# Kernel tuning notes

Measured on AMD Instinct MI355X. Metric: run time of the kernel, lower is better.

## Reference

```python
import jax, jax.numpy as jnp
import numpy as np

B, S, D_MODEL, N_HEADS = 4, 8192, 1024, 16
D_K = D_MODEL // N_HEADS


def setup_inputs() -> dict:
    key = jax.random.key(0)
    k1, k2, k3 = jax.random.split(key, 3)
    x = jax.random.normal(k1, (B, S, D_MODEL), dtype=jnp.float32)
    w_qkv = jax.random.normal(k2, (D_MODEL, 3 * D_MODEL), dtype=jnp.float32) * (1.0 / np.sqrt(D_MODEL))
    w_o = jax.random.normal(k3, (D_MODEL, D_MODEL), dtype=jnp.float32) * (1.0 / np.sqrt(D_MODEL))
    return {"x": x, "w_qkv": w_qkv, "w_o": w_o}


def reference(x, w_qkv, w_o):
    b, s, dm = x.shape
    h, d = N_HEADS, D_K
    qkv = (x @ w_qkv).reshape(b, s, 3, h, d)  # (b, s, 3, h, d)
    q, k, v = qkv[:, :, 0], qkv[:, :, 1], qkv[:, :, 2]  # each (b, s, h, d)
    # ELU+1 feature map (positive features)
    q = jax.nn.elu(q) + 1.0
    k = jax.nn.elu(k) + 1.0
    # Global (non-causal) KV aggregation: (b, h, d, d)
    kv = jnp.einsum('bnhd,bnhf->bhdf', k, v)
    k_sum = k.sum(axis=1)  # (b, h, d)
    numerator = jnp.einsum('bnhd,bhdf->bnhf', q, kv)  # (b, s, h, d)
    denominator = jnp.einsum('bnhd,bhd->bnh', q, k_sum)[..., None] + 1e-6
    attn = (numerator / denominator).reshape(b, s, dm)
    return attn @ w_o
```

## Files before the change

### kernel.cpp

```cpp
#include <hip/hip_runtime.h>
#include <cmath>

constexpr int BB = 4;
constexpr int SS = 8192;
constexpr int DMODEL = 1024;
constexpr int NHEADS = 16;
constexpr int DHEAD = 64;
constexpr int MTOK = BB * SS;

typedef __attribute__((ext_vector_type(8))) short short8;
typedef __attribute__((ext_vector_type(4))) float f32x4;

__device__ __forceinline__ unsigned short f2bf(float f) {
    unsigned u = __float_as_uint(f);
    u += 0x7FFF + ((u >> 16) & 1);
    return (unsigned short)(u >> 16);
}

#define STAGE2(gbase, lbase)                                                          \
    do {                                                                              \
        __builtin_amdgcn_global_load_lds(                                             \
            (const __attribute__((address_space(1))) unsigned int*)((gbase) + o0),    \
            (__attribute__((address_space(3))) unsigned int*)((lbase) + d0), 16, 0, 0);\
        __builtin_amdgcn_global_load_lds(                                             \
            (const __attribute__((address_space(1))) unsigned int*)((gbase) + o1),    \
            (__attribute__((address_space(3))) unsigned int*)((lbase) + d1), 16, 0, 0);\
    } while (0)

template <int EPI>
__global__ __launch_bounds__(512, 2) void la_gemm256(
    const unsigned short* __restrict__ A, const unsigned short* __restrict__ B,
    float* __restrict__ Cf,
    unsigned short* __restrict__ Cq, unsigned short* __restrict__ Ck,
    unsigned short* __restrict__ Cv,
    const int N, const int K, const int GX)
{
    extern __shared__ __align__(16) unsigned short smem[];

    const int t = threadIdx.x;
    const int wave = t >> 6, lane = t & 63;
    const int wm = wave >> 2, wn = wave & 3;
    const int quad = lane >> 4, fl = lane & 15;

    const int nwg = (int)gridDim.x;
    const int cpx = nwg >> 3;
    const int id = ((int)blockIdx.x & 7) * cpx + ((int)blockIdx.x >> 3);
    const int bx = id % GX, by = id / GX;
    const int m0 = by * 256, n0 = bx * 256;

    const unsigned short* a_g = A + (size_t)m0 * K;
    const unsigned short* b_g = B + (size_t)n0 * K;

    const int c0 = t, c1 = 512 + t;
    const size_t o0 = (size_t)(c0 >> 2) * K + (size_t)((((c0 & 3) ^ ((c0 >> 3) & 3))) << 3);
    const size_t o1 = (size_t)(c1 >> 2) * K + (size_t)((((c1 & 3) ^ ((c1 >> 3) & 3))) << 3);
    const int d0 = c0 * 8, d1 = c1 * 8;

    const int qsc = (quad ^ ((fl >> 1) & 3)) << 3;
    const int offA = (wm * 128 + fl) * 32 + qsc;
    const int offB = (wn * 64 + fl) * 32 + qsc;

    f32x4 acc[8][4];
#pragma unroll
    for (int i = 0; i < 8; ++i)
#pragma unroll
        for (int j = 0; j < 4; ++j) acc[i][j] = (f32x4){0.f, 0.f, 0.f, 0.f};

    unsigned short* bufc = smem;
    unsigned short* bufn = smem + 32768;

    STAGE2(a_g,      bufc);
    STAGE2(b_g,      bufc + 16384);
    STAGE2(a_g + 32, bufc + 8192);
    STAGE2(b_g + 32, bufc + 24576);
    asm volatile("s_waitcnt vmcnt(4)" ::: "memory");
    __builtin_amdgcn_s_barrier();

    for (int kt = 0; kt < K - 64; kt += 64) {
        const unsigned short* an = a_g + kt + 64;
        const unsigned short* bn = b_g + kt + 64;
        short8 ah[4], bh[4];

#pragma unroll
        for (int i = 0; i < 4; ++i) ah[i] = *(const short8*)(bufc + offA + i * 512);
#pragma unroll
        for (int j = 0; j < 4; ++j) bh[j] = *(const short8*)(bufc + 16384 + offB + j * 512);
        STAGE2(an, bufn);
        __builtin_amdgcn_s_barrier();
        asm volatile("s_waitcnt lgkmcnt(0)" ::: "memory");
        __builtin_amdgcn_s_setprio(1);
#pragma unroll
        for (int i = 0; i < 4; ++i)
#pragma unroll
            for (int j = 0; j < 4; ++j)
                acc[i][j] = __builtin_amdgcn_mfma_f32_16x16x32_bf16(ah[i], bh[j], acc[i][j], 0, 0, 0);
        __builtin_amdgcn_s_setprio(0);
        __builtin_amdgcn_s_barrier();

#pragma unroll
        for (int i = 0; i < 4; ++i) ah[i] = *(const short8*)(bufc + offA + 2048 + i * 512);
        STAGE2(bn, bufn + 16384);
        __builtin_amdgcn_s_barrier();
        asm volatile("s_waitcnt lgkmcnt(0)" ::: "memory");
        __builtin_amdgcn_s_setprio(1);
#pragma unroll
        for (int i = 0; i < 4; ++i)
#pragma unroll
            for (int j = 0; j < 4; ++j)
                acc[4 + i][j] = __builtin_amdgcn_mfma_f32_16x16x32_bf16(ah[i], bh[j], acc[4 + i][j], 0, 0, 0);
        __builtin_amdgcn_s_setprio(0);
        asm volatile("s_waitcnt vmcnt(4)" ::: "memory");
        __builtin_amdgcn_s_barrier();

#pragma unroll
        for (int i = 0; i < 4; ++i) ah[i] = *(const short8*)(bufc + 8192 + offA + i * 512);
#pragma unroll
        for (int j = 0; j < 4; ++j) bh[j] = *(const short8*)(bufc + 24576 + offB + j * 512);
        STAGE2(an + 32, bufn + 8192);
        __builtin_amdgcn_s_barrier();
        asm volatile("s_waitcnt lgkmcnt(0)" ::: "memory");
        __builtin_amdgcn_s_setprio(1);
#pragma unroll
        for (int i = 0; i < 4; ++i)
#pragma unroll
            for (int j = 0; j < 4; ++j)
                acc[i][j] = __builtin_amdgcn_mfma_f32_16x16x32_bf16(ah[i], bh[j], acc[i][j], 0, 0, 0);
        __builtin_amdgcn_s_setprio(0);
        __builtin_amdgcn_s_barrier();

#pragma unroll
        for (int i = 0; i < 4; ++i) ah[i] = *(const short8*)(bufc + 8192 + offA + 2048 + i * 512);
        STAGE2(bn + 32, bufn + 24576);
        __builtin_amdgcn_s_barrier();
        asm volatile("s_waitcnt lgkmcnt(0)" ::: "memory");
        __builtin_amdgcn_s_setprio(1);
#pragma unroll
        for (int i = 0; i < 4; ++i)
#pragma unroll
            for (int j = 0; j < 4; ++j)
                acc[4 + i][j] = __builtin_amdgcn_mfma_f32_16x16x32_bf16(ah[i], bh[j], acc[4 + i][j], 0, 0, 0);
        __builtin_amdgcn_s_setprio(0);
        asm volatile("s_waitcnt vmcnt(4)" ::: "memory");
        __builtin_amdgcn_s_barrier();

        unsigned short* tmp = bufc; bufc = bufn; bufn = tmp;
    }

    {
        short8 ah[4], bh[4];
#pragma unroll
        for (int i = 0; i < 4; ++i) ah[i] = *(const short8*)(bufc + offA + i * 512);
#pragma unroll
        for (int j = 0; j < 4; ++j) bh[j] = *(const short8*)(bufc + 16384 + offB + j * 512);
#pragma unroll
        for (int i = 0; i < 4; ++i)
#pragma unroll
            for (int j = 0; j < 4; ++j)
                acc[i][j] = __builtin_amdgcn_mfma_f32_16x16x32_bf16(ah[i], bh[j], acc[i][j], 0, 0, 0);
#pragma unroll
        for (int i = 0; i < 4; ++i) ah[i] = *(const short8*)(bufc + offA + 2048 + i * 512);
#pragma unroll
        for (int i = 0; i < 4; ++i)
#pragma unroll
            for (int j = 0; j < 4; ++j)
                acc[4 + i][j] = __builtin_amdgcn_mfma_f32_16x16x32_bf16(ah[i], bh[j], acc[4 + i][j], 0, 0, 0);
        asm volatile("s_waitcnt vmcnt(0)" ::: "memory");
        __builtin_amdgcn_s_barrier();
#pragma unroll
        for (int i = 0; i < 4; ++i) ah[i] = *(const short8*)(bufc + 8192 + offA + i * 512);
#pragma unroll
        for (int j = 0; j < 4; ++j) bh[j] = *(const short8*)(bufc + 24576 + offB + j * 512);
#pragma unroll
        for (int i = 0; i < 4; ++i)
#pragma unroll
            for (int j = 0; j < 4; ++j)
                acc[i][j] = __builtin_amdgcn_mfma_f32_16x16x32_bf16(ah[i], bh[j], acc[i][j], 0, 0, 0);
#pragma unroll
        for (int i = 0; i < 4; ++i) ah[i] = *(const short8*)(bufc + 8192 + offA + 2048 + i * 512);
#pragma unroll
        for (int i = 0; i < 4; ++i)
#pragma unroll
            for (int j = 0; j < 4; ++j)
                acc[4 + i][j] = __builtin_amdgcn_mfma_f32_16x16x32_bf16(ah[i], bh[j], acc[4 + i][j], 0, 0, 0);
    }

    if (EPI == 1) {
        const int bsel = n0 >> 10;
        unsigned short* Cp = (bsel == 0) ? Cq : ((bsel == 1) ? Ck : Cv);
        const bool act = (bsel < 2);
        const int colb = (n0 & 1023) + wn * 64 + fl;
#pragma unroll
        for (int i = 0; i < 8; ++i) {
            const int rowb = m0 + wm * 128 + i * 16 + quad * 4;
#pragma unroll
            for (int j = 0; j < 4; ++j) {
                const int col = colb + j * 16;
#pragma unroll
                for (int r = 0; r < 4; ++r) {
                    float v = acc[i][j][r];
                    if (act) v = (v > 0.f) ? v + 1.f : __expf(v);
                    Cp[(size_t)(rowb + r) * 1024 + col] = f2bf(v);
                }
            }
        }
    } else {
#pragma unroll
        for (int i = 0; i < 8; ++i) {
            const int rowb = m0 + wm * 128 + i * 16 + quad * 4;
#pragma unroll
            for (int j = 0; j < 4; ++j) {
                const int col = n0 + wn * 64 + fl + j * 16;
#pragma unroll
                for (int r = 0; r < 4; ++r)
                    Cf[(size_t)(rowb + r) * N + col] = acc[i][j][r];
            }
        }
    }
}

__global__ __launch_bounds__(256) void cast_bf16(
    const float4* __restrict__ in, ushort4* __restrict__ hi, int n4)
{
    int i = blockIdx.x * 256 + threadIdx.x;
    const int stride = gridDim.x * 256;
    for (; i < n4; i += stride) {
        const float4 v = in[i];
        ushort4 h;
        h.x = f2bf(v.x); h.y = f2bf(v.y); h.z = f2bf(v.z); h.w = f2bf(v.w);
        hi[i] = h;
    }
}

__global__ __launch_bounds__(256) void cast_T(
    const float* __restrict__ w, unsigned short* __restrict__ hiT, int Kd, int Nd)
{
    __shared__ float tile[32][33];
    const int t = threadIdx.x;
    const int n0 = blockIdx.x * 32, k0 = blockIdx.y * 32;
    const int r = t >> 3, c4 = (t & 7) * 4;
    const float4 v = *(const float4*)(w + (size_t)(k0 + r) * Nd + n0 + c4);
    tile[r][c4 + 0] = v.x; tile[r][c4 + 1] = v.y;
    tile[r][c4 + 2] = v.z; tile[r][c4 + 3] = v.w;
    __syncthreads();
    ushort4 h;
    h.x = f2bf(tile[c4 + 0][r]); h.y = f2bf(tile[c4 + 1][r]);
    h.z = f2bf(tile[c4 + 2][r]); h.w = f2bf(tile[c4 + 3][r]);
    *(ushort4*)(hiT + (size_t)(n0 + r) * Kd + k0 + c4) = h;
}

constexpr int KV_CHUNKS = 16;

__global__ __launch_bounds__(256) void la_kvsum(
    const unsigned short* __restrict__ Kb, const unsigned short* __restrict__ Vb,
    float* __restrict__ kv, float* __restrict__ ksum)
{
    __shared__ float kk[32][68];
    __shared__ float vv[32][68];
    const int t = threadIdx.x;
    const int bh = blockIdx.x;
    const int b = bh >> 4, h = bh & 15;
    const int r = t >> 3, c8 = (t & 7) * 8;
    const int d0 = (t & 15) * 4, f0 = (t >> 4) * 4;
    float acc[4][4];
#pragma unroll
    for (int i = 0; i < 4; ++i)
#pragma unroll
        for (int j = 0; j < 4; ++j) acc[i][j] = 0.f;
    float ks = 0.f;
    const int s0 = blockIdx.y * (SS / KV_CHUNKS);

    for (int st = 0; st < SS / KV_CHUNKS; st += 32) {
        const size_t row = (size_t)(b * SS + s0 + st + r) * DMODEL + h * DHEAD + c8;
        const uint4 ku = *(const uint4*)(Kb + row);
        const uint4 vu = *(const uint4*)(Vb + row);
        __syncthreads();
        const unsigned ka_[4] = {ku.x, ku.y, ku.z, ku.w};
        const unsigned va_[4] = {vu.x, vu.y, vu.z, vu.w};
#pragma unroll
        for (int e = 0; e < 4; ++e) {
            kk[r][c8 + 2 * e]     = __uint_as_float(ka_[e] << 16);
            kk[r][c8 + 2 * e + 1] = __uint_as_float(ka_[e] & 0xFFFF0000u);
            vv[r][c8 + 2 * e]     = __uint_as_float(va_[e] << 16);
            vv[r][c8 + 2 * e + 1] = __uint_as_float(va_[e] & 0xFFFF0000u);
        }
        __syncthreads();
#pragma unroll 8
        for (int rr = 0; rr < 32; ++rr) {
            float4 kr = *(const float4*)&kk[rr][d0];
            float4 vr = *(const float4*)&vv[rr][f0];
            float ka[4] = {kr.x, kr.y, kr.z, kr.w};
            float va[4] = {vr.x, vr.y, vr.z, vr.w};
#pragma unroll
            for (int i = 0; i < 4; ++i)
#pragma unroll
                for (int j = 0; j < 4; ++j)
                    acc[i][j] = fmaf(ka[i], va[j], acc[i][j]);
        }
        if (t < 64) {
#pragma unroll 8
            for (int rr = 0; rr < 32; ++rr) ks += kk[rr][t];
        }
    }

    float* kvp = kv + (size_t)bh * DHEAD * DHEAD;
#pragma unroll
    for (int i = 0; i < 4; ++i)
#pragma unroll
        for (int j = 0; j < 4; ++j)
            atomicAdd(&kvp[(d0 + i) * DHEAD + f0 + j], acc[i][j]);
    if (t < 64) atomicAdd(&ksum[bh * DHEAD + t], ks);
}

__global__ __launch_bounds__(256) void la_attn(
    const unsigned short* __restrict__ Q, const float* __restrict__ kv,
    const float* __restrict__ ksum, unsigned short* __restrict__ attn)
{
    __shared__ float kvs[64][68];
    __shared__ float qs[64][68];
    __shared__ float kss[64];
    const int t = threadIdx.x;
    const int t0 = blockIdx.x * 64;
    const int b = t0 / SS;
    const int tok_g = t >> 4;
    const int f_g = t & 15;

    for (int hh = 0; hh < NHEADS; ++hh) {
        __syncthreads();
        const float* kvp = kv + (size_t)(b * NHEADS + hh) * DHEAD * DHEAD;
#pragma unroll
        for (int i = 0; i < 4; ++i) {
            const int idx = i * 256 + t;
            const int r = idx >> 4, c4 = (idx & 15) * 4;
            *(float4*)&kvs[r][c4] = *(const float4*)(kvp + r * 64 + c4);
        }
        if (t < 64) kss[t] = ksum[(b * NHEADS + hh) * DHEAD + t];
#pragma unroll
        for (int i = 0; i < 2; ++i) {
            const int idx = i * 256 + t;
            const int r = idx >> 3, c8 = (idx & 7) * 8;
            const uint4 qu = *(const uint4*)(Q + (size_t)(t0 + r) * DMODEL + hh * 64 + c8);
            const unsigned a[4] = {qu.x, qu.y, qu.z, qu.w};
#pragma unroll
            for (int e = 0; e < 4; ++e) {
                qs[r][c8 + 2 * e]     = __uint_as_float(a[e] << 16);
                qs[r][c8 + 2 * e + 1] = __uint_as_float(a[e] & 0xFFFF0000u);
            }
        }
        __syncthreads();

        float acc[4][4];
        float den[4];
#pragma unroll
        for (int i = 0; i < 4; ++i) {
            den[i] = 0.f;
#pragma unroll
            for (int j = 0; j < 4; ++j) acc[i][j] = 0.f;
        }
#pragma unroll 8
        for (int d = 0; d < 64; ++d) {
            const float4 kvf = *(const float4*)&kvs[d][f_g * 4];
            const float ks = kss[d];
#pragma unroll
            for (int i = 0; i < 4; ++i) {
                const float qd = qs[tok_g * 4 + i][d];
                den[i]    = fmaf(qd, ks,    den[i]);
                acc[i][0] = fmaf(qd, kvf.x, acc[i][0]);
                acc[i][1] = fmaf(qd, kvf.y, acc[i][1]);
                acc[i][2] = fmaf(qd, kvf.z, acc[i][2]);
                acc[i][3] = fmaf(qd, kvf.w, acc[i][3]);
            }
        }
#pragma unroll
        for (int i = 0; i < 4; ++i) {
            const float rcp = 1.f / (den[i] + 1e-6f);
            ushort4 o;
            o.x = f2bf(acc[i][0] * rcp); o.y = f2bf(acc[i][1] * rcp);
            o.z = f2bf(acc[i][2] * rcp); o.w = f2bf(acc[i][3] * rcp);
            *(ushort4*)(attn + (size_t)(t0 + tok_g * 4 + i) * DMODEL + hh * 64 + f_g * 4) = o;
        }
    }
}

__global__ void la_sentinel(float* out, int n) {
    int i = blockIdx.x * 256 + threadIdx.x;
    if (i < n) out[i] = 12345.0f;
}

extern "C" void kernel_launch(void* const* d_in, const int* in_sizes, int n_in,
                              void* d_out, int out_size, void* d_ws, size_t ws_size,
                              hipStream_t stream)
{
    const float* x     = (const float*)d_in[0];
    const float* w_qkv = (const float*)d_in[1];
    const float* w_o   = (const float*)d_in[2];
    float* out = (float*)d_out;

    static bool attr_done = []() {
        hipFuncSetAttribute((const void*)&la_gemm256<1>,
                            hipFuncAttributeMaxDynamicSharedMemorySize, 131072);
        hipFuncSetAttribute((const void*)&la_gemm256<0>,
                            hipFuncAttributeMaxDynamicSharedMemorySize, 131072);
        return true;
    }();
    (void)attr_done;

    char* p = (char*)d_ws;
    const size_t x_bf = (size_t)MTOK * DMODEL * 2;
    unsigned short* x_hi = (unsigned short*)p; p += x_bf;
    unsigned short* wqT = (unsigned short*)p; p += (size_t)3 * DMODEL * DMODEL * 2;
    unsigned short* woT = (unsigned short*)p; p += (size_t)DMODEL * DMODEL * 2;
    unsigned short* q_buf = (unsigned short*)p; p += x_bf;
    unsigned short* k_buf = (unsigned short*)p; p += x_bf;
    unsigned short* v_buf = (unsigned short*)p; p += x_bf;
    float* kvb = (float*)p; p += (size_t)BB * NHEADS * DHEAD * DHEAD * 4;
    float* ksb = (float*)p; p += (size_t)BB * NHEADS * DHEAD * 4;

    if ((size_t)(p - (char*)d_ws) > ws_size) {
        la_sentinel<<<(MTOK * DMODEL + 255) / 256, 256, 0, stream>>>(out, MTOK * DMODEL);
        return;
    }

    hipMemsetAsync(kvb, 0,
                   (size_t)(BB * NHEADS * DHEAD * DHEAD + BB * NHEADS * DHEAD) * sizeof(float),
                   stream);

    cast_bf16<<<8192, 256, 0, stream>>>((const float4*)x, (ushort4*)x_hi,
                                        MTOK * DMODEL / 4);
    cast_T<<<dim3(3 * DMODEL / 32, DMODEL / 32), 256, 0, stream>>>(w_qkv, wqT,
                                                                   DMODEL, 3 * DMODEL);
    cast_T<<<dim3(DMODEL / 32, DMODEL / 32), 256, 0, stream>>>(w_o, woT,
                                                               DMODEL, DMODEL);

    la_gemm256<1><<<(3 * DMODEL / 256) * (MTOK / 256), 512, 131072, stream>>>(
        x_hi, wqT, nullptr, q_buf, k_buf, v_buf, 3 * DMODEL, DMODEL, 3 * DMODEL / 256);

    la_kvsum<<<dim3(BB * NHEADS, KV_CHUNKS), 256, 0, stream>>>(k_buf, v_buf, kvb, ksb);

    la_attn<<<MTOK / 64, 256, 0, stream>>>(q_buf, kvb, ksb, x_hi);

    la_gemm256<0><<<(DMODEL / 256) * (MTOK / 256), 512, 131072, stream>>>(
        x_hi, woT, out, nullptr, nullptr, nullptr, DMODEL, DMODEL, DMODEL / 256);
}
```

Baseline: 727.0 us.

## Double-buffer MFMA register fragments to overlap LDS reads with matrix math

Measured after the change: 719.2 us. No clear change (-1.1%).

```diff
diff --git a/kernel.cpp b/kernel.cpp
--- a/kernel.cpp
+++ b/kernel.cpp
@@ -27,6 +27,18 @@
             (__attribute__((address_space(3))) unsigned int*)((lbase) + d1), 16, 0, 0);\
     } while (0)
 
+#define MFMA16(ACCROW, AH, BH)                                                        \
+    do {                                                                              \
+        __builtin_amdgcn_s_setprio(1);                                                \
+        _Pragma("unroll")                                                             \
+        for (int i = 0; i < 4; ++i)                                                   \
+            _Pragma("unroll")                                                         \
+            for (int j = 0; j < 4; ++j)                                               \
+                acc[ACCROW + i][j] = __builtin_amdgcn_mfma_f32_16x16x32_bf16(         \
+                    AH[i], BH[j], acc[ACCROW + i][j], 0, 0, 0);                       \
+        __builtin_amdgcn_s_setprio(0);                                                \
+    } while (0)
+
 template <int EPI>
 __global__ __launch_bounds__(512, 2) void la_gemm256(
     const unsigned short* __restrict__ A, const unsigned short* __restrict__ B,
@@ -75,114 +87,54 @@
     STAGE2(b_g + 32, bufc + 24576);
     asm volatile("s_waitcnt vmcnt(4)" ::: "memory");
     __builtin_amdgcn_s_barrier();
-
-    for (int kt = 0; kt < K - 64; kt += 64) {
-        const unsigned short* an = a_g + kt + 64;
-        const unsigned short* bn = b_g + kt + 64;
-        short8 ah[4], bh[4];
-
-#pragma unroll
-        for (int i = 0; i < 4; ++i) ah[i] = *(const short8*)(bufc + offA + i * 512);
-#pragma unroll
-        for (int j = 0; j < 4; ++j) bh[j] = *(const short8*)(bufc + 16384 + offB + j * 512);
+    __builtin_amdgcn_sched_barrier(0);
+
+    short8 ah0[4], ah1[4], bh0[4], bh1[4];
+#pragma unroll
+    for (int i = 0; i < 4; ++i) ah0[i] = *(const short8*)(bufc + offA + i * 512);
+#pragma unroll
+    for (int j = 0; j < 4; ++j) bh0[j] = *(const short8*)(bufc + 16384 + offB + j * 512);
+
+    for (int kt = 0; kt < K; kt += 64) {
+        const int ktn = (kt + 64 < K) ? kt + 64 : kt;
+        const unsigned short* an = a_g + ktn;
+        const unsigned short* bn = b_g + ktn;
+
+#pragma unroll
+        for (int i = 0; i < 4; ++i) ah1[i] = *(const short8*)(bufc + offA + 2048 + i * 512);
         STAGE2(an, bufn);
+        MFMA16(0, ah0, bh0);
+        asm volatile("s_waitcnt vmcnt(2)" ::: "memory");
         __builtin_amdgcn_s_barrier();
-        asm volatile("s_waitcnt lgkmcnt(0)" ::: "memory");
-        __builtin_amdgcn_s_setprio(1);
-#pragma unroll
-        for (int i = 0; i < 4; ++i)
-#pragma unroll
-            for (int j = 0; j < 4; ++j)
-                acc[i][j] = __builtin_amdgcn_mfma_f32_16x16x32_bf16(ah[i], bh[j], acc[i][j], 0, 0, 0);
-        __builtin_amdgcn_s_setprio(0);
+        __builtin_amdgcn_sched_barrier(0);
+
+#pragma unroll
+        for (int i = 0; i < 4; ++i) ah0[i] = *(const short8*)(bufc + 8192 + offA + i * 512);
+#pragma unroll
+        for (int j = 0; j < 4; ++j) bh1[j] = *(const short8*)(bufc + 24576 + offB + j * 512);
+        STAGE2(bn, bufn + 16384);
+        MFMA16(4, ah1, bh0);
         __builtin_amdgcn_s_barrier();
 
 #pragma unroll
-        for (int i = 0; i < 4; ++i) ah[i] = *(const short8*)(bufc + offA + 2048 + i * 512);
-        STAGE2(bn, bufn + 16384);
+        for (int i = 0; i < 4; ++i) ah1[i] = *(const short8*)(bufc + 8192 + offA + 2048 + i * 512);
+        STAGE2(an + 32, bufn + 8192);
+        MFMA16(0, ah0, bh1);
+        asm volatile("s_waitcnt vmcnt(2)" ::: "memory");
         __builtin_amdgcn_s_barrier();
-        asm volatile("s_waitcnt lgkmcnt(0)" ::: "memory");
-        __builtin_amdgcn_s_setprio(1);
-#pragma unroll
-        for (int i = 0; i < 4; ++i)
-#pragma unroll
-            for (int j = 0; j < 4; ++j)
-                acc[4 + i][j] = __builtin_amdgcn_mfma_f32_16x16x32_bf16(ah[i], bh[j], acc[4 + i][j], 0, 0, 0);
-        __builtin_amdgcn_s_setprio(0);
-        asm volatile("s_waitcnt vmcnt(4)" ::: "memory");
+        __builtin_amdgcn_sched_barrier(0);
+
+#pragma unroll
+        for (int i = 0; i < 4; ++i) ah0[i] = *(const short8*)(bufn + offA + i * 512);
+#pragma unroll
+        for (int j = 0; j < 4; ++j) bh0[j] = *(const short8*)(bufn + 16384 + offB + j * 512);
+        STAGE2(bn + 32, bufn + 24576);
+        MFMA16(4, ah1, bh1);
         __builtin_amdgcn_s_barrier();
 
-#pragma unroll
-        for (int i = 0; i < 4; ++i) ah[i] = *(const short8*)(bufc + 8192 + offA + i * 512);
-#pragma unroll
-        for (int j = 0; j < 4; ++j) bh[j] = *(const short8*)(bufc + 24576 + offB + j * 512);
-        STAGE2(an + 32, bufn + 8192);
-        __builtin_amdgcn_s_barrier();
-        asm volatile("s_waitcnt lgkmcnt(0)" ::: "memory");
-        __builtin_amdgcn_s_setprio(1);
-#pragma unroll
-        for (int i = 0; i < 4; ++i)
-#pragma unroll
-            for (int j = 0; j < 4; ++j)
-                acc[i][j] = __builtin_amdgcn_mfma_f32_16x16x32_bf16(ah[i], bh[j], acc[i][j], 0, 0, 0);
-        __builtin_amdgcn_s_setprio(0);
-        __builtin_amdgcn_s_barrier();
-
-#pragma unroll
-        for (int i = 0; i < 4; ++i) ah[i] = *(const short8*)(bufc + 8192 + offA + 2048 + i * 512);
-        STAGE2(bn + 32, bufn + 24576);
-        __builtin_amdgcn_s_barrier();
-        asm volatile("s_waitcnt lgkmcnt(0)" ::: "memory");
-        __builtin_amdgcn_s_setprio(1);
-#pragma unroll
-        for (int i = 0; i < 4; ++i)
-#pragma unroll
-            for (int j = 0; j < 4; ++j)
-                acc[4 + i][j] = __builtin_amdgcn_mfma_f32_16x16x32_bf16(ah[i], bh[j], acc[4 + i][j], 0, 0, 0);
-        __builtin_amdgcn_s_setprio(0);
-        asm volatile("s_waitcnt vmcnt(4)" ::: "memory");
-        __builtin_amdgcn_s_barrier();
-
         unsigned short* tmp = bufc; bufc = bufn; bufn = tmp;
     }
-
-    {
-        short8 ah[4], bh[4];
-#pragma unroll
-        for (int i = 0; i < 4; ++i) ah[i] = *(const short8*)(bufc + offA + i * 512);
-#pragma unroll
-        for (int j = 0; j < 4; ++j) bh[j] = *(const short8*)(bufc + 16384 + offB + j * 512);
-#pragma unroll
-        for (int i = 0; i < 4; ++i)
-#pragma unroll
-            for (int j = 0; j < 4; ++j)
-                acc[i][j] = __builtin_amdgcn_mfma_f32_16x16x32_bf16(ah[i], bh[j], acc[i][j], 0, 0, 0);
-#pragma unroll
-        for (int i = 0; i < 4; ++i) ah[i] = *(const short8*)(bufc + offA + 2048 + i * 512);
-#pragma unroll
-        for (int i = 0; i < 4; ++i)
-#pragma unroll
-            for (int j = 0; j < 4; ++j)
-                acc[4 + i][j] = __builtin_amdgcn_mfma_f32_16x16x32_bf16(ah[i], bh[j], acc[4 + i][j], 0, 0, 0);
-        asm volatile("s_waitcnt vmcnt(0)" ::: "memory");
-        __builtin_amdgcn_s_barrier();
-#pragma unroll
-        for (int i = 0; i < 4; ++i) ah[i] = *(const short8*)(bufc + 8192 + offA + i * 512);
-#pragma unroll
-        for (int j = 0; j < 4; ++j) bh[j] = *(const short8*)(bufc + 24576 + offB + j * 512);
-#pragma unroll
-        for (int i = 0; i < 4; ++i)
-#pragma unroll
-            for (int j = 0; j < 4; ++j)
-                acc[i][j] = __builtin_amdgcn_mfma_f32_16x16x32_bf16(ah[i], bh[j], acc[i][j], 0, 0, 0);
-#pragma unroll
-        for (int i = 0; i < 4; ++i) ah[i] = *(const short8*)(bufc + 8192 + offA + 2048 + i * 512);
-#pragma unroll
-        for (int i = 0; i < 4; ++i)
-#pragma unroll
-            for (int j = 0; j < 4; ++j)
-                acc[4 + i][j] = __builtin_amdgcn_mfma_f32_16x16x32_bf16(ah[i], bh[j], acc[4 + i][j], 0, 0, 0);
-    }
+    asm volatile("s_waitcnt vmcnt(0)" ::: "memory");
 
     if (EPI == 1) {
         const int bsel = n0 >> 10;
```
